# Kernel tuning notes

Measured on AMD Instinct MI355X. Metric: run time of the kernel, lower is better.

The kernel has to match this reference:

```python
import jax, jax.numpy as jnp
import numpy as np

DIM = 512
NUM_HEADS = 8
HEAD_DIM = DIM // NUM_HEADS
SCALE = HEAD_DIM ** -0.5


def setup_inputs() -> dict:
    key = jax.random.key(0)
    ks = jax.random.split(key, 11)
    B, T, D = 2, 4096, DIM
    s = 0.02
    return {
        "query": jax.random.normal(ks[0], (B, T, D), jnp.float32),
        "key_": jax.random.normal(ks[1], (B, T, D), jnp.float32),
        "value": jax.random.normal(ks[2], (B, T, D), jnp.float32),
        "Wq": jax.random.normal(ks[3], (D, D), jnp.float32) * s,
        "bq": jnp.zeros((D,), jnp.float32),
        "Wk": jax.random.normal(ks[4], (D, D), jnp.float32) * s,
        "bk": jnp.zeros((D,), jnp.float32),
        "Wv": jax.random.normal(ks[5], (D, D), jnp.float32) * s,
        "bv": jnp.zeros((D,), jnp.float32),
        "Wo": jax.random.normal(ks[6], (D, D), jnp.float32) * s,
        "bo": jnp.zeros((D,), jnp.float32),
    }


def reference(query, key_, value, Wq, bq, Wk, bk, Wv, bv, Wo, bo):
    B, T, D = query.shape
    H, Hd = NUM_HEADS, HEAD_DIM
    # Linear projections (torch Linear: x @ W.T + b)
    q = (query @ Wq.T + bq).reshape(B, T, H, Hd).transpose(0, 2, 1, 3)   # [B,H,T,Hd]
    k = (key_ @ Wk.T + bk).reshape(B, -1, H, Hd).transpose(0, 2, 1, 3)    # [B,H,S,Hd]
    v = (value @ Wv.T + bv).reshape(B, -1, H, Hd).transpose(0, 2, 1, 3)   # [B,H,S,Hd]
    # Full O(T*S) score matrix, as in the original (non-fused) module
    scores = jnp.einsum("bhtd,bhsd->bhts", q, k) * SCALE                  # [B,H,T,S]
    weights = jax.nn.softmax(scores, axis=-1)
    out = jnp.einsum("bhts,bhsd->bhtd", weights, v)                       # [B,H,T,Hd]
    out = out.transpose(0, 2, 1, 3).reshape(B, T, D)
    return out @ Wo.T + bo
```

## Files before the change

kernel.cpp:

```cpp
#include <hip/hip_runtime.h>
#include <cstdint>
#include <cstddef>

typedef __attribute__((ext_vector_type(8)))  __bf16 bf16x8;
typedef __attribute__((ext_vector_type(4)))  float  f32x4;
typedef __attribute__((ext_vector_type(16))) float  f32x16;
typedef __attribute__((ext_vector_type(8)))  unsigned short us8;

#define MFMA(a, b, c)   __builtin_amdgcn_mfma_f32_16x16x32_bf16((a), (b), (c), 0, 0, 0)
#define MFMA32(a, b, c) __builtin_amdgcn_mfma_f32_32x32x16_bf16((a), (b), (c), 0, 0, 0)

#define QSCALE 0.18033688011112042f

__device__ __forceinline__ unsigned short f2bf(float f) {
  unsigned u = __float_as_uint(f);
  u += 0x7fffu + ((u >> 16) & 1u);
  return (unsigned short)(u >> 16);
}

__device__ __forceinline__ unsigned pk2bf(float lo, float hi) {
  unsigned a = __float_as_uint(lo) + 0x8000u;
  unsigned b = __float_as_uint(hi) + 0x8000u;
  return __builtin_amdgcn_perm(b, a, 0x07060302u);
}

__device__ __forceinline__ void gload16(const void* g, void* l) {
  __builtin_amdgcn_global_load_lds(
      (__attribute__((address_space(1))) unsigned int*)(uintptr_t)g,
      (__attribute__((address_space(3))) unsigned int*)l,
      16, 0, 0);
}

struct CastArgs {
  const float*    src[7];
  unsigned short* dst[7];
  int             n4[7];
};
__global__ __launch_bounds__(256) void cast_kernel(CastArgs a) {
  int z = blockIdx.y;
  const float* __restrict__ in = a.src[z];
  unsigned short* __restrict__ out = a.dst[z];
  int i = blockIdx.x * 256 + threadIdx.x;
  if (i < a.n4[z]) {
    float4 f = ((const float4*)in)[i];
    ushort4 r;
    r.x = f2bf(f.x); r.y = f2bf(f.y); r.z = f2bf(f.z); r.w = f2bf(f.w);
    ((ushort4*)out)[i] = r;
  }
}

struct ProjArgs {
  const unsigned short* X[3];
  const unsigned short* W[3];
  const float*          bias[3];
  unsigned short*       out[3];
};

__global__ __launch_bounds__(256) void proj_qkv_kernel(ProjArgs args) {
  __shared__ alignas(16) unsigned short smem[16384];

  const int z = blockIdx.z;
  const unsigned short* __restrict__ X   = args.X[z];
  const unsigned short* __restrict__ W   = args.W[z];
  const float* __restrict__ bias         = args.bias[z];
  unsigned short* __restrict__ out       = args.out[z];
  const float scl = (z == 0) ? QSCALE : 1.0f;

  const int t = threadIdx.x;
  const int w = t >> 6, lane = t & 63;
  const int quad = lane >> 4, l15 = lane & 15;
  const int wr = w >> 1, wc = w & 1;
  const int m0 = blockIdx.x * 128, n0 = blockIdx.y * 128;

  const int srow = t >> 2;
  const int scol = (((t & 3) ^ (srow & 3)) << 3);

  f32x4 acc[4][4] = {};

  {
    unsigned short* sA = smem;
    unsigned short* sB = smem + 4096;
    gload16(X + (size_t)(m0 + srow) * 512 + scol,      &sA[w * 512]);
    gload16(X + (size_t)(m0 + srow + 64) * 512 + scol, &sA[2048 + w * 512]);
    gload16(W + (size_t)(n0 + srow) * 512 + scol,      &sB[w * 512]);
    gload16(W + (size_t)(n0 + srow + 64) * 512 + scol, &sB[2048 + w * 512]);
  }

  for (int k0 = 0; k0 < 512; k0 += 32) {
    const int buf = (k0 >> 5) & 1;
    unsigned short* sA = smem + buf * 8192;
    unsigned short* sB = sA + 4096;
    if (k0 < 480) {
      unsigned short* nA = smem + (buf ^ 1) * 8192;
      unsigned short* nB = nA + 4096;
      const int kn = k0 + 32;
      gload16(X + (size_t)(m0 + srow) * 512 + kn + scol,      &nA[w * 512]);
      gload16(X + (size_t)(m0 + srow + 64) * 512 + kn + scol, &nA[2048 + w * 512]);
      gload16(W + (size_t)(n0 + srow) * 512 + kn + scol,      &nB[w * 512]);
      gload16(W + (size_t)(n0 + srow + 64) * 512 + kn + scol, &nB[2048 + w * 512]);
      asm volatile("s_waitcnt vmcnt(4)" ::: "memory");
    } else {
      asm volatile("s_waitcnt vmcnt(0)" ::: "memory");
    }
    __builtin_amdgcn_s_barrier();
    asm volatile("" ::: "memory");

    bf16x8 af[4], bfr[4];
#pragma unroll
    for (int mt = 0; mt < 4; ++mt) {
      int ra = wr * 64 + mt * 16 + l15;
      af[mt] = *(const bf16x8*)&sA[ra * 32 + ((quad ^ (ra & 3)) << 3)];
    }
#pragma unroll
    for (int nt = 0; nt < 4; ++nt) {
      int rb = wc * 64 + nt * 16 + l15;
      bfr[nt] = *(const bf16x8*)&sB[rb * 32 + ((quad ^ (rb & 3)) << 3)];
    }
#pragma unroll
    for (int mt = 0; mt < 4; ++mt)
#pragma unroll
      for (int nt = 0; nt < 4; ++nt)
        acc[mt][nt] = MFMA(af[mt], bfr[nt], acc[mt][nt]);

    asm volatile("" ::: "memory");
    __builtin_amdgcn_s_barrier();
  }

  if (z != 2) {
#pragma unroll
    for (int nt = 0; nt < 4; ++nt) {
      int n = n0 + wc * 64 + nt * 16 + l15;
      float bv = bias[n];
      int h = n >> 6, hd = n & 63;
#pragma unroll
      for (int mt = 0; mt < 4; ++mt) {
#pragma unroll
        for (int r = 0; r < 4; ++r) {
          int m = m0 + wr * 64 + mt * 16 + quad * 4 + r;
          int b = m >> 12, tt = m & 4095;
          out[(((size_t)(b * 8 + h)) * 4096 + tt) * 64 + hd] =
              f2bf((acc[mt][nt][r] + bv) * scl);
        }
      }
    }
  } else {
    const int b   = m0 >> 12;
    const int tt0 = m0 & 4095;
#pragma unroll
    for (int h2 = 0; h2 < 2; ++h2) {
      __syncthreads();
      if (wc == h2) {
#pragma unroll
        for (int nt = 0; nt < 4; ++nt) {
          int nl = nt * 16 + l15;
          float bv = bias[n0 + h2 * 64 + nl];
#pragma unroll
          for (int mt = 0; mt < 4; ++mt)
#pragma unroll
            for (int r = 0; r < 4; ++r) {
              int ml = wr * 64 + mt * 16 + quad * 4 + r;
              smem[nl * 136 + ml] = f2bf((acc[mt][nt][r] + bv) * scl);
            }
        }
      }
      __syncthreads();
      const int row = t >> 2;
      const int c4  = (t & 3) * 8;
      const int n   = n0 + h2 * 64 + row;
      unsigned short* dst = out + ((size_t)(b * 512 + n)) * 4096 + tt0;
#pragma unroll
      for (int k = 0; k < 4; ++k)
        *(us8*)(dst + c4 + k * 32) = *(const us8*)&smem[row * 136 + c4 + k * 32];
    }
  }
}

__global__ __launch_bounds__(256) void proj_out_kernel(
    const unsigned short* __restrict__ X, const unsigned short* __restrict__ W,
    const float* __restrict__ bias, float* __restrict__ out) {
  __shared__ alignas(16) unsigned short smem[16384];

  const int t = threadIdx.x;
  const int w = t >> 6, lane = t & 63;
  const int quad = lane >> 4, l15 = lane & 15;
  const int wr = w >> 1, wc = w & 1;
  const int m0 = blockIdx.x * 128, n0 = blockIdx.y * 128;
  const int srow = t >> 2;
  const int scol = (((t & 3) ^ (srow & 3)) << 3);

  f32x4 acc[4][4] = {};

  {
    unsigned short* sA = smem;
    unsigned short* sB = smem + 4096;
    gload16(X + (size_t)(m0 + srow) * 512 + scol,      &sA[w * 512]);
    gload16(X + (size_t)(m0 + srow + 64) * 512 + scol, &sA[2048 + w * 512]);
    gload16(W + (size_t)(n0 + srow) * 512 + scol,      &sB[w * 512]);
    gload16(W + (size_t)(n0 + srow + 64) * 512 + scol, &sB[2048 + w * 512]);
  }

  for (int k0 = 0; k0 < 512; k0 += 32) {
    const int buf = (k0 >> 5) & 1;
    unsigned short* sA = smem + buf * 8192;
    unsigned short* sB = sA + 4096;
    if (k0 < 480) {
      unsigned short* nA = smem + (buf ^ 1) * 8192;
      unsigned short* nB = nA + 4096;
      const int kn = k0 + 32;
      gload16(X + (size_t)(m0 + srow) * 512 + kn + scol,      &nA[w * 512]);
      gload16(X + (size_t)(m0 + srow + 64) * 512 + kn + scol, &nA[2048 + w * 512]);
      gload16(W + (size_t)(n0 + srow) * 512 + kn + scol,      &nB[w * 512]);
      gload16(W + (size_t)(n0 + srow + 64) * 512 + kn + scol, &nB[2048 + w * 512]);
      asm volatile("s_waitcnt vmcnt(4)" ::: "memory");
    } else {
      asm volatile("s_waitcnt vmcnt(0)" ::: "memory");
    }
    __builtin_amdgcn_s_barrier();
    asm volatile("" ::: "memory");

    bf16x8 af[4], bfr[4];
#pragma unroll
    for (int mt = 0; mt < 4; ++mt) {
      int ra = wr * 64 + mt * 16 + l15;
      af[mt] = *(const bf16x8*)&sA[ra * 32 + ((quad ^ (ra & 3)) << 3)];
    }
#pragma unroll
    for (int nt = 0; nt < 4; ++nt) {
      int rb = wc * 64 + nt * 16 + l15;
      bfr[nt] = *(const bf16x8*)&sB[rb * 32 + ((quad ^ (rb & 3)) << 3)];
    }
#pragma unroll
    for (int mt = 0; mt < 4; ++mt)
#pragma unroll
      for (int nt = 0; nt < 4; ++nt)
        acc[mt][nt] = MFMA(af[mt], bfr[nt], acc[mt][nt]);

    asm volatile("" ::: "memory");
    __builtin_amdgcn_s_barrier();
  }

#pragma unroll
  for (int nt = 0; nt < 4; ++nt) {
    int n = n0 + wc * 64 + nt * 16 + l15;
    float bv = bias[n];
#pragma unroll
    for (int mt = 0; mt < 4; ++mt) {
#pragma unroll
      for (int r = 0; r < 4; ++r) {
        int m = m0 + wr * 64 + mt * 16 + quad * 4 + r;
        out[(size_t)m * 512 + n] = acc[mt][nt][r] + bv;
      }
    }
  }
}

__global__ __launch_bounds__(256, 2) void attn_kernel(
    const unsigned short* __restrict__ Q, const unsigned short* __restrict__ K,
    const unsigned short* __restrict__ VT, unsigned short* __restrict__ Aout) {
  __shared__ alignas(16) unsigned short kt[2][8192];
  __shared__ alignas(16) unsigned short vt[2][8192];

  const int t = threadIdx.x;
  const int w = t >> 6, lane = t & 63;
  const int l31 = lane & 31, h = lane >> 5;

  const int wg  = blockIdx.x + gridDim.x * blockIdx.y;
  const int swz = (wg & 7) * 64 + (wg >> 3);
  const int bx = swz & 31, bh = swz >> 5;

  const unsigned short* __restrict__ Qp  = Q  + (size_t)bh * 4096 * 64;
  const unsigned short* __restrict__ Kp  = K  + (size_t)bh * 4096 * 64;
  const unsigned short* __restrict__ VTp = VT + (size_t)bh * 64 * 4096;

  const int q0w = bx * 128 + w * 32;

  const int grow = t >> 3;
  const int gcol = (((t & 7) ^ (grow & 7)) << 3);
  const int vr4  = w * 4 + ((t & 63) >> 4);
  const int vcol = (((t & 15) ^ vr4) << 3);

#define STAGE(bbuf, s0)                                                        \
  {                                                                            \
    _Pragma("unroll")                                                          \
    for (int i = 0; i < 4; ++i)                                                \
      gload16(Kp + (size_t)((s0) + grow + 32 * i) * 64 + gcol,                 \
              &kt[bbuf][i * 2048 + w * 512]);                                  \
    _Pragma("unroll")                                                          \
    for (int i = 0; i < 4; ++i)                                                \
      gload16(VTp + (size_t)(i * 16 + vr4) * 4096 + (s0) + vcol,               \
              &vt[bbuf][(i * 16 + w * 4) * 128]);                              \
  }

  STAGE(0, 0);

  bf16x8 aq[4];
#pragma unroll
  for (int kd = 0; kd < 4; ++kd)
    aq[kd] = *(const bf16x8*)(Qp + (size_t)(q0w + l31) * 64 + kd * 16 + h * 8);

  union { unsigned short s[8]; bf16x8 v; } one_u;
#pragma unroll
  for (int i = 0; i < 8; ++i) one_u.s[i] = 0x3F80;
  const bf16x8 ones = one_u.v;

  f32x16 o0 = {}, o1 = {}, lsum = {};

  const int swzk = (l31 & 7) << 3;
  const int swzv = (l31 & 15);

  for (int j = 0; j < 32; ++j) {
    const int cb = j & 1, nb = cb ^ 1;
    if (j < 31) {
      STAGE(nb, (j + 1) * 128);
      asm volatile("s_waitcnt vmcnt(8)" ::: "memory");
    } else {
      asm volatile("s_waitcnt vmcnt(0)" ::: "memory");
    }
    __builtin_amdgcn_s_barrier();
    asm volatile("" ::: "memory");

    const unsigned short* ktb = kt[cb];
    const unsigned short* vtb = vt[cb];

#pragma unroll
    for (int st = 0; st < 4; ++st) {
      f32x16 scv = {};
#pragma unroll
      for (int kd = 0; kd < 4; ++kd) {
        bf16x8 kf = *(const bf16x8*)&ktb[(st * 32 + l31) * 64 +
                                         ((((2 * kd + h) << 3)) ^ swzk)];
        scv = MFMA32(kf, aq[kd], scv);
      }

      float p[16];
#pragma unroll
      for (int r = 0; r < 16; ++r) p[r] = __builtin_amdgcn_exp2f(scv[r]);
      unsigned Xg[4], Yg[4];
#pragma unroll
      for (int g = 0; g < 4; ++g) {
        Xg[g] = pk2bf(p[4 * g + 0], p[4 * g + 1]);
        Yg[g] = pk2bf(p[4 * g + 2], p[4 * g + 3]);
      }

#pragma unroll
      for (int ks = 0; ks < 2; ++ks) {
        unsigned Lx = h ? Xg[2 * ks + 1] : Xg[2 * ks];
        unsigned Mx = h ? Xg[2 * ks]     : Xg[2 * ks + 1];
        unsigned Ly = h ? Yg[2 * ks + 1] : Yg[2 * ks];
        unsigned My = h ? Yg[2 * ks]     : Yg[2 * ks + 1];
        unsigned sMx = (unsigned)__shfl_xor((int)Mx, 32, 64);
        unsigned sMy = (unsigned)__shfl_xor((int)My, 32, 64);
        union { unsigned u[4]; bf16x8 v; } pa;
        pa.u[0] = h ? sMx : Lx;
        pa.u[1] = h ? sMy : Ly;
        pa.u[2] = h ? Lx  : sMx;
        pa.u[3] = h ? Ly  : sMy;
        const int c = st * 4 + 2 * ks + h;
        bf16x8 v0 = *(const bf16x8*)&vtb[l31 * 128 + ((c ^ swzv) << 3)];
        bf16x8 v1 = *(const bf16x8*)&vtb[(l31 + 32) * 128 + ((c ^ swzv) << 3)];
        o0 = MFMA32(pa.v, v0, o0);
        o1 = MFMA32(pa.v, v1, o1);
        lsum = MFMA32(pa.v, ones, lsum);
      }
    }

    asm volatile("" ::: "memory");
    __builtin_amdgcn_s_barrier();
  }
#undef STAGE

  const int bq = bh >> 3, hh = bh & 7;
#pragma unroll
  for (int r = 0; r < 16; ++r) {
    const int qloc = (r & 3) + 8 * (r >> 2) + 4 * h;
    const float inv = 1.0f / lsum[r];
    const int trow = q0w + qloc;
    const size_t base = ((size_t)bq * 4096 + trow) * 512 + hh * 64;
    Aout[base + l31]      = f2bf(o0[r] * inv);
    Aout[base + 32 + l31] = f2bf(o1[r] * inv);
  }
}

extern "C" void kernel_launch(void* const* d_in, const int* in_sizes, int n_in,
                              void* d_out, int out_size, void* d_ws, size_t ws_size,
                              hipStream_t stream) {
  (void)in_sizes; (void)n_in; (void)out_size; (void)ws_size;
  const float* query = (const float*)d_in[0];
  const float* key_  = (const float*)d_in[1];
  const float* value = (const float*)d_in[2];
  const float* Wq = (const float*)d_in[3];
  const float* bq = (const float*)d_in[4];
  const float* Wk = (const float*)d_in[5];
  const float* bk = (const float*)d_in[6];
  const float* Wv = (const float*)d_in[7];
  const float* bv = (const float*)d_in[8];
  const float* Wo = (const float*)d_in[9];
  const float* bo = (const float*)d_in[10];
  float* out = (float*)d_out;

  char* ws = (char*)d_ws;
  const size_t MB = 1024 * 1024;
  unsigned short* Xq  = (unsigned short*)(ws + 0 * MB);
  unsigned short* Xk  = (unsigned short*)(ws + 8 * MB);
  unsigned short* Xv  = (unsigned short*)(ws + 16 * MB);
  unsigned short* Wqb = (unsigned short*)(ws + 24 * MB);
  unsigned short* Wkb = (unsigned short*)(ws + 24 * MB + 512 * 1024);
  unsigned short* Wvb = (unsigned short*)(ws + 25 * MB);
  unsigned short* Wob = (unsigned short*)(ws + 25 * MB + 512 * 1024);
  unsigned short* qb  = (unsigned short*)(ws + 26 * MB);
  unsigned short* kb  = (unsigned short*)(ws + 34 * MB);
  unsigned short* vtb = (unsigned short*)(ws + 42 * MB);
  unsigned short* ao  = Xq;

  CastArgs ca;
  ca.src[0] = query; ca.src[1] = key_; ca.src[2] = value;
  ca.src[3] = Wq;    ca.src[4] = Wk;   ca.src[5] = Wv;  ca.src[6] = Wo;
  ca.dst[0] = Xq;    ca.dst[1] = Xk;   ca.dst[2] = Xv;
  ca.dst[3] = Wqb;   ca.dst[4] = Wkb;  ca.dst[5] = Wvb; ca.dst[6] = Wob;
  ca.n4[0] = ca.n4[1] = ca.n4[2] = 1048576;
  ca.n4[3] = ca.n4[4] = ca.n4[5] = ca.n4[6] = 65536;
  cast_kernel<<<dim3(4096, 7), 256, 0, stream>>>(ca);

  ProjArgs pa;
  pa.X[0] = Xq;  pa.X[1] = Xk;  pa.X[2] = Xv;
  pa.W[0] = Wqb; pa.W[1] = Wkb; pa.W[2] = Wvb;
  pa.bias[0] = bq; pa.bias[1] = bk; pa.bias[2] = bv;
  pa.out[0] = qb; pa.out[1] = kb; pa.out[2] = vtb;
  proj_qkv_kernel<<<dim3(64, 4, 3), 256, 0, stream>>>(pa);

  attn_kernel<<<dim3(32, 16), 256, 0, stream>>>(qb, kb, vtb, ao);

  proj_out_kernel<<<dim3(64, 4), 256, 0, stream>>>(ao, Wob, bo, out);
}
```

Baseline: 231.1 us.

## Split attention over key halves with a combine kernel for more parallelism

New measurement: 240.4 us. +4.0%, slower.

```diff
diff --git a/kernel.cpp b/kernel.cpp
--- a/kernel.cpp
+++ b/kernel.cpp
@@ -16,6 +16,11 @@
   unsigned u = __float_as_uint(f);
   u += 0x7fffu + ((u >> 16) & 1u);
   return (unsigned short)(u >> 16);
+}
+
+__device__ __forceinline__ float bf2f(unsigned short s) {
+  unsigned u = ((unsigned)s) << 16;
+  return __uint_as_float(u);
 }
 
 __device__ __forceinline__ unsigned pk2bf(float lo, float hi) {
@@ -254,44 +259,45 @@
   }
 }
 
-__global__ __launch_bounds__(256, 2) void attn_kernel(
+__global__ __launch_bounds__(256, 4) void attn_kernel(
     const unsigned short* __restrict__ Q, const unsigned short* __restrict__ K,
-    const unsigned short* __restrict__ VT, unsigned short* __restrict__ Aout) {
-  __shared__ alignas(16) unsigned short kt[2][8192];
-  __shared__ alignas(16) unsigned short vt[2][8192];
+    const unsigned short* __restrict__ VT,
+    unsigned short* __restrict__ pO0, unsigned short* __restrict__ pO1,
+    float* __restrict__ pL) {
+  __shared__ alignas(16) unsigned short kt[2][4096];
+  __shared__ alignas(16) unsigned short vt[2][4096];
 
   const int t = threadIdx.x;
   const int w = t >> 6, lane = t & 63;
   const int l31 = lane & 31, h = lane >> 5;
 
   const int wg  = blockIdx.x + gridDim.x * blockIdx.y;
-  const int swz = (wg & 7) * 64 + (wg >> 3);
-  const int bx = swz & 31, bh = swz >> 5;
+  const int swz = (wg & 7) * 128 + (wg >> 3);
+  const int bx  = swz & 31;
+  const int bh2 = swz >> 5;
+  const int bh  = bh2 & 15, half = bh2 >> 4;
 
   const unsigned short* __restrict__ Qp  = Q  + (size_t)bh * 4096 * 64;
   const unsigned short* __restrict__ Kp  = K  + (size_t)bh * 4096 * 64;
   const unsigned short* __restrict__ VTp = VT + (size_t)bh * 64 * 4096;
 
   const int q0w = bx * 128 + w * 32;
+  const int sbase = half * 2048;
 
   const int grow = t >> 3;
   const int gcol = (((t & 7) ^ (grow & 7)) << 3);
-  const int vr4  = w * 4 + ((t & 63) >> 4);
-  const int vcol = (((t & 15) ^ vr4) << 3);
 
 #define STAGE(bbuf, s0)                                                        \
   {                                                                            \
-    _Pragma("unroll")                                                          \
-    for (int i = 0; i < 4; ++i)                                                \
-      gload16(Kp + (size_t)((s0) + grow + 32 * i) * 64 + gcol,                 \
-              &kt[bbuf][i * 2048 + w * 512]);                                  \
-    _Pragma("unroll")                                                          \
-    for (int i = 0; i < 4; ++i)                                                \
-      gload16(VTp + (size_t)(i * 16 + vr4) * 4096 + (s0) + vcol,               \
-              &vt[bbuf][(i * 16 + w * 4) * 128]);                              \
-  }
-
-  STAGE(0, 0);
+    gload16(Kp + (size_t)((s0) + grow) * 64 + gcol,        &kt[bbuf][w * 512]);\
+    gload16(Kp + (size_t)((s0) + grow + 32) * 64 + gcol,                       \
+            &kt[bbuf][2048 + w * 512]);                                        \
+    gload16(VTp + (size_t)grow * 4096 + (s0) + gcol,       &vt[bbuf][w * 512]);\
+    gload16(VTp + (size_t)(grow + 32) * 4096 + (s0) + gcol,                    \
+            &vt[bbuf][2048 + w * 512]);                                        \
+  }
+
+  STAGE(0, sbase);
 
   bf16x8 aq[4];
 #pragma unroll
@@ -305,14 +311,13 @@
 
   f32x16 o0 = {}, o1 = {}, lsum = {};
 
-  const int swzk = (l31 & 7) << 3;
-  const int swzv = (l31 & 15);
+  const int swzk = (l31 & 7);
 
   for (int j = 0; j < 32; ++j) {
     const int cb = j & 1, nb = cb ^ 1;
     if (j < 31) {
-      STAGE(nb, (j + 1) * 128);
-      asm volatile("s_waitcnt vmcnt(8)" ::: "memory");
+      STAGE(nb, sbase + (j + 1) * 64);
+      asm volatile("s_waitcnt vmcnt(4)" ::: "memory");
     } else {
       asm volatile("s_waitcnt vmcnt(0)" ::: "memory");
     }
@@ -323,12 +328,12 @@
     const unsigned short* vtb = vt[cb];
 
 #pragma unroll
-    for (int st = 0; st < 4; ++st) {
+    for (int st = 0; st < 2; ++st) {
       f32x16 scv = {};
 #pragma unroll
       for (int kd = 0; kd < 4; ++kd) {
         bf16x8 kf = *(const bf16x8*)&ktb[(st * 32 + l31) * 64 +
-                                         ((((2 * kd + h) << 3)) ^ swzk)];
+                                         (((2 * kd + h) ^ swzk) << 3)];
         scv = MFMA32(kf, aq[kd], scv);
       }
 
@@ -356,8 +361,9 @@
         pa.u[2] = h ? Lx  : sMx;
         pa.u[3] = h ? Ly  : sMy;
         const int c = st * 4 + 2 * ks + h;
-        bf16x8 v0 = *(const bf16x8*)&vtb[l31 * 128 + ((c ^ swzv) << 3)];
-        bf16x8 v1 = *(const bf16x8*)&vtb[(l31 + 32) * 128 + ((c ^ swzv) << 3)];
+        bf16x8 v0 = *(const bf16x8*)&vtb[l31 * 64 + ((c ^ swzk) << 3)];
+        bf16x8 v1 = *(const bf16x8*)&vtb[(l31 + 32) * 64 +
+                                         ((c ^ ((l31 + 32) & 7)) << 3)];
         o0 = MFMA32(pa.v, v0, o0);
         o1 = MFMA32(pa.v, v1, o1);
         lsum = MFMA32(pa.v, ones, lsum);
@@ -369,16 +375,37 @@
   }
 #undef STAGE
 
+  unsigned short* __restrict__ PO = half ? pO1 : pO0;
+  float* __restrict__ PLh = pL + half * 65536 + bh * 4096;
   const int bq = bh >> 3, hh = bh & 7;
 #pragma unroll
   for (int r = 0; r < 16; ++r) {
     const int qloc = (r & 3) + 8 * (r >> 2) + 4 * h;
-    const float inv = 1.0f / lsum[r];
     const int trow = q0w + qloc;
     const size_t base = ((size_t)bq * 4096 + trow) * 512 + hh * 64;
-    Aout[base + l31]      = f2bf(o0[r] * inv);
-    Aout[base + 32 + l31] = f2bf(o1[r] * inv);
-  }
+    PO[base + l31]      = f2bf(o0[r]);
+    PO[base + 32 + l31] = f2bf(o1[r]);
+    if (l31 == 0) PLh[trow] = lsum[r];
+  }
+}
+
+__global__ __launch_bounds__(256) void combine_kernel(
+    const unsigned short* __restrict__ p0, const unsigned short* __restrict__ p1,
+    const float* __restrict__ pL, unsigned short* __restrict__ ao) {
+  const int i = blockIdx.x * 256 + threadIdx.x;
+  const int idx8 = i * 8;
+  const int col = idx8 & 511;
+  const int t   = (idx8 >> 9) & 4095;
+  const int bq  = idx8 >> 21;
+  const int bh  = bq * 8 + (col >> 6);
+  const float inv = 1.0f / (pL[bh * 4096 + t] + pL[65536 + bh * 4096 + t]);
+  us8 a = *(const us8*)&p0[idx8];
+  us8 b = *(const us8*)&p1[idx8];
+  us8 o;
+#pragma unroll
+  for (int k = 0; k < 8; ++k)
+    o[k] = f2bf((bf2f(a[k]) + bf2f(b[k])) * inv);
+  *(us8*)&ao[idx8] = o;
 }
 
 extern "C" void kernel_launch(void* const* d_in, const int* in_sizes, int n_in,
@@ -406,11 +433,14 @@
   unsigned short* Wqb = (unsigned short*)(ws + 24 * MB);
   unsigned short* Wkb = (unsigned short*)(ws + 24 * MB + 512 * 1024);
   unsigned short* Wvb = (unsigned short*)(ws + 25 * MB);
-  unsigned short* Wob = (unsigned short*)(ws + 25 * MB + 512 * 1024);
   unsigned short* qb  = (unsigned short*)(ws + 26 * MB);
   unsigned short* kb  = (unsigned short*)(ws + 34 * MB);
   unsigned short* vtb = (unsigned short*)(ws + 42 * MB);
-  unsigned short* ao  = Xq;
+  unsigned short* Wob = (unsigned short*)(ws + 58 * MB);
+  unsigned short* pO0 = (unsigned short*)(ws + 0 * MB);
+  unsigned short* pO1 = (unsigned short*)(ws + 9 * MB);
+  float*          pL  = (float*)(ws + 18 * MB);
+  unsigned short* ao  = (unsigned short*)(ws + 42 * MB);
 
   CastArgs ca;
   ca.src[0] = query; ca.src[1] = key_; ca.src[2] = value;
@@ -428,7 +458,9 @@
   pa.out[0] = qb; pa.out[1] = kb; pa.out[2] = vtb;
   proj_qkv_kernel<<<dim3(64, 4, 3), 256, 0, stream>>>(pa);
 
-  attn_kernel<<<dim3(32, 16), 256, 0, stream>>>(qb, kb, vtb, ao);
+  attn_kernel<<<dim3(32, 32), 256, 0, stream>>>(qb, kb, vtb, pO0, pO1, pL);
+
+  combine_kernel<<<dim3(2048), 256, 0, stream>>>(pO0, pO1, pL, ao);
 
   proj_out_kernel<<<dim3(64, 4), 256, 0, stream>>>(ao, Wob, bo, out);
 }
```
